# Optimization experiments

Measured on AMD Instinct MI355X. Metric: run time of the kernel, lower is better.

The kernel has to match this reference:

```python
import jax, jax.numpy as jnp
import numpy as np

N, E, D, C = 10000, 160000, 2500, 16


def setup_inputs() -> dict:
    key = jax.random.key(0)
    ks = jax.random.split(key, 12)
    s = 1.0 / np.sqrt(D)
    inp = {
        "x": jax.random.normal(ks[0], (N, D), dtype=jnp.float32),
        "edge_index": jax.random.randint(ks[1], (2, E), 0, N, dtype=jnp.int64),
        # SAGEConv 1 (mean aggregator): out = x @ W_self + mean_neigh @ W_neigh + b
        "W1_self": jax.random.normal(ks[2], (D, D), dtype=jnp.float32) * s,
        "W1_neigh": jax.random.normal(ks[3], (D, D), dtype=jnp.float32) * s,
        "b1": jnp.zeros((D,), dtype=jnp.float32),
        # SAGEConv 2
        "W2_self": jax.random.normal(ks[4], (D, D), dtype=jnp.float32) * s,
        "W2_neigh": jax.random.normal(ks[5], (D, D), dtype=jnp.float32) * s,
        "b2": jnp.zeros((D,), dtype=jnp.float32),
        # classifier: Linear(D, D) -> ReLU -> Linear(D, C)
        "Wc1": jax.random.normal(ks[6], (D, D), dtype=jnp.float32) * s,
        "bc1": jnp.zeros((D,), dtype=jnp.float32),
        "Wc2": jax.random.normal(ks[7], (D, C), dtype=jnp.float32) * s,
        "bc2": jnp.zeros((C,), dtype=jnp.float32),
    }
    return inp


def _sage_conv(h, src, dst, W_self, W_neigh, b):
    # mean aggregation over in-neighbors (messages flow src -> dst)
    agg = jax.ops.segment_sum(h[src], dst, num_segments=N)          # [N, D]
    deg = jax.ops.segment_sum(jnp.ones((src.shape[0],), h.dtype), dst, num_segments=N)
    mean = agg / jnp.maximum(deg, 1.0)[:, None]
    return h @ W_self + mean @ W_neigh + b


def reference(x, edge_index, W1_self, W1_neigh, b1, W2_self, W2_neigh, b2,
              Wc1, bc1, Wc2, bc2):
    src, dst = edge_index[0], edge_index[1]
    h = jax.nn.relu(_sage_conv(x, src, dst, W1_self, W1_neigh, b1))
    h = jax.nn.relu(_sage_conv(h, src, dst, W2_self, W2_neigh, b2))
    h = jax.nn.relu(h @ Wc1 + bc1)
    return h @ Wc2 + bc2  # [N, num_classes]
```

## Files before the change

kernel.cpp:

```cpp
#include <hip/hip_runtime.h>
#include <stdint.h>

#define NNODES 10000
#define NEDGES 160000
#define DIM    2500
#define NCLS   16
#define KP     2560
#define MP     10240
#define K2     5120
#define GN     20
#define KT_SEG 40

typedef __attribute__((ext_vector_type(8))) short short8;
typedef __attribute__((ext_vector_type(4))) float f32x4;
typedef __attribute__((address_space(3))) void as3_void;
typedef const __attribute__((address_space(1))) void as1_cvoid;

__device__ __forceinline__ unsigned short f2bf(float f) {
    unsigned u = __float_as_uint(f);
    u += 0x7FFFu + ((u >> 16) & 1u);
    return (unsigned short)(u >> 16);
}
__device__ __forceinline__ float bf2f(unsigned short s) {
    return __uint_as_float(((unsigned)s) << 16);
}

__global__ void k_deg(const int* __restrict__ ei, int* __restrict__ deg) {
    int e = blockIdx.x * blockDim.x + threadIdx.x;
    if (e < NEDGES) atomicAdd(&deg[ei[NEDGES + e]], 1);
}

__global__ void k_scan(const int* __restrict__ deg, int* __restrict__ off) {
    __shared__ int s[1024];
    __shared__ int carryS;
    int t = threadIdx.x;
    if (t == 0) carryS = 0;
    __syncthreads();
    for (int c = 0; c < NNODES; c += 1024) {
        int i = c + t;
        int v = (i < NNODES) ? deg[i] : 0;
        s[t] = v;
        __syncthreads();
        for (int o = 1; o < 1024; o <<= 1) {
            int add = (t >= o) ? s[t - o] : 0;
            __syncthreads();
            s[t] += add;
            __syncthreads();
        }
        int base = carryS;
        if (i < NNODES) off[i] = base + s[t] - v;
        __syncthreads();
        if (t == 1023) carryS += s[1023];
        __syncthreads();
    }
    if (t == 0) off[NNODES] = carryS;
}

__global__ void k_fill(const int* __restrict__ ei, const int* __restrict__ off,
                       int* __restrict__ cur, int* __restrict__ csr) {
    int e = blockIdx.x * blockDim.x + threadIdx.x;
    if (e < NEDGES) {
        int s = ei[e];
        int d = ei[NEDGES + e];
        int p = atomicAdd(&cur[d], 1);
        csr[off[d] + p] = s;
    }
}

__global__ void k_cvt_x(const float* __restrict__ x,
                        unsigned short* __restrict__ hi, unsigned short* __restrict__ lo) {
    long long idx = (long long)blockIdx.x * blockDim.x + threadIdx.x;
    const int C4 = KP / 4;
    if (idx >= (long long)MP * C4) return;
    int row = (int)(idx / C4), c4 = (int)(idx % C4);
    int k = c4 * 4;
    float vv[4] = {0.f, 0.f, 0.f, 0.f};
    if (row < NNODES && k < DIM) {
        float4 v = *(const float4*)(x + (size_t)row * DIM + k);
        vv[0] = v.x; vv[1] = v.y; vv[2] = v.z; vv[3] = v.w;
    }
    unsigned hw[2], lw[2];
    for (int j = 0; j < 2; j++) {
        unsigned short h0 = f2bf(vv[2*j]);     unsigned short l0 = f2bf(vv[2*j]   - bf2f(h0));
        unsigned short h1 = f2bf(vv[2*j+1]);   unsigned short l1 = f2bf(vv[2*j+1] - bf2f(h1));
        hw[j] = (unsigned)h0 | ((unsigned)h1 << 16);
        lw[j] = (unsigned)l0 | ((unsigned)l1 << 16);
    }
    *(uint2*)(hi + (size_t)row * KP + k) = make_uint2(hw[0], hw[1]);
    *(uint2*)(lo + (size_t)row * KP + k) = make_uint2(lw[0], lw[1]);
}

__global__ __launch_bounds__(320) void k_agg(
    const unsigned short* __restrict__ shi, const unsigned short* __restrict__ slo,
    const int* __restrict__ off, const int* __restrict__ csr, const int* __restrict__ deg,
    unsigned short* __restrict__ mhi, unsigned short* __restrict__ mlo) {
    int d = blockIdx.x;
    int t = threadIdx.x;
    int s0 = off[d], s1 = off[d + 1];
    float acc[8];
    #pragma unroll
    for (int i = 0; i < 8; i++) acc[i] = 0.f;
    for (int e = s0; e < s1; e++) {
        int s = csr[e];
        uint4 hv = *((const uint4*)(shi + (size_t)s * KP) + t);
        uint4 lv = *((const uint4*)(slo + (size_t)s * KP) + t);
        unsigned hu[4] = {hv.x, hv.y, hv.z, hv.w};
        unsigned lu[4] = {lv.x, lv.y, lv.z, lv.w};
        #pragma unroll
        for (int j = 0; j < 4; j++) {
            acc[2*j]   += bf2f((unsigned short)(hu[j] & 0xFFFFu)) + bf2f((unsigned short)(lu[j] & 0xFFFFu));
            acc[2*j+1] += bf2f((unsigned short)(hu[j] >> 16))     + bf2f((unsigned short)(lu[j] >> 16));
        }
    }
    int dg = deg[d];
    float inv = 1.0f / (float)(dg > 1 ? dg : 1);
    unsigned oh[4], ol[4];
    #pragma unroll
    for (int j = 0; j < 4; j++) {
        float m0 = acc[2*j] * inv, m1 = acc[2*j+1] * inv;
        unsigned short h0 = f2bf(m0); unsigned short l0 = f2bf(m0 - bf2f(h0));
        unsigned short h1 = f2bf(m1); unsigned short l1 = f2bf(m1 - bf2f(h1));
        oh[j] = (unsigned)h0 | ((unsigned)h1 << 16);
        ol[j] = (unsigned)l0 | ((unsigned)l1 << 16);
    }
    *((uint4*)(mhi + (size_t)d * KP) + t) = make_uint4(oh[0], oh[1], oh[2], oh[3]);
    *((uint4*)(mlo + (size_t)d * KP) + t) = make_uint4(ol[0], ol[1], ol[2], ol[3]);
}

__global__ __launch_bounds__(256) void k_cvt_w(const float* __restrict__ W,
                                               unsigned short* __restrict__ wth,
                                               unsigned short* __restrict__ wtl, int seg) {
    __shared__ float tile[64][65];
    int k0 = blockIdx.x * 64, n0 = blockIdx.y * 64;
    int t = threadIdx.x;
    for (int j = 0; j < 16; j++) {
        int lin = t + j * 256;
        int kk = lin >> 6, nn = lin & 63;
        int gk = k0 + kk, gn = n0 + nn;
        tile[kk][nn] = (gk < DIM && gn < DIM) ? W[(size_t)gk * DIM + gn] : 0.f;
    }
    __syncthreads();
    for (int j = 0; j < 16; j++) {
        int lin = t + j * 256;
        int nn = lin >> 6, kk = lin & 63;
        float v = tile[kk][nn];
        unsigned short h = f2bf(v);
        unsigned short l = f2bf(v - bf2f(h));
        size_t o = (size_t)(n0 + nn) * K2 + (size_t)seg * KP + (k0 + kk);
        wth[o] = h;
        wtl[o] = l;
    }
}

__global__ __launch_bounds__(256, 2) void k_gemm(
    const unsigned short* __restrict__ AsH, const unsigned short* __restrict__ AsL,
    const unsigned short* __restrict__ AmH, const unsigned short* __restrict__ AmL,
    const unsigned short* __restrict__ BH,  const unsigned short* __restrict__ BL,
    const float* __restrict__ bias,
    unsigned short* __restrict__ OH, unsigned short* __restrict__ OL, int ktiles) {
    __shared__ __align__(16) unsigned short lds[4 * 128 * 64];
    const int tid = threadIdx.x;
    const int wave = tid >> 6, lane = tid & 63;
    const int g = blockIdx.x;
    const int tm = g / GN, tn = g % GN;

    const int srow = tid >> 3;
    const int sc = (tid & 7) ^ (srow & 7);
    size_t aOff[4], bOff[4];
    #pragma unroll
    for (int j = 0; j < 4; j++) {
        int row = j * 32 + srow;
        aOff[j] = (size_t)(tm * 128 + row) * KP + sc * 8;
        bOff[j] = (size_t)(tn * 128 + row) * K2 + sc * 8;
    }
    char* ldsB = (char*)lds;
    const int dstBase = wave * 1024;

    const int wr = wave >> 1, wc = wave & 1;
    const int frow = lane & 15, fk = lane >> 4;
    int aFo[2][4], bFo[2][4];
    #pragma unroll
    for (int s = 0; s < 2; s++) {
        #pragma unroll
        for (int i = 0; i < 4; i++) {
            int ra = wr * 64 + i * 16 + frow;
            aFo[s][i] = ra * 64 + (((s * 4 + fk) ^ (ra & 7)) * 8);
            int rb = wc * 64 + i * 16 + frow;
            bFo[s][i] = rb * 64 + (((s * 4 + fk) ^ (rb & 7)) * 8);
        }
    }

    f32x4 acc[4][4];
    #pragma unroll
    for (int i = 0; i < 4; i++)
        #pragma unroll
        for (int j = 0; j < 4; j++) acc[i][j] = (f32x4){0.f, 0.f, 0.f, 0.f};

    for (int kt = 0; kt < ktiles; kt++) {
        const unsigned short *Ah, *Al;
        int kA;
        if (kt < KT_SEG) { Ah = AsH; Al = AsL; kA = kt * 64; }
        else             { Ah = AmH; Al = AmL; kA = (kt - KT_SEG) * 64; }
        const int kB = kt * 64;
        #pragma unroll
        for (int j = 0; j < 4; j++) {
            __builtin_amdgcn_global_load_lds((as1_cvoid*)(Ah + aOff[j] + kA),
                (as3_void*)(ldsB + 0 * 16384 + j * 4096 + dstBase), 16, 0, 0);
            __builtin_amdgcn_global_load_lds((as1_cvoid*)(Al + aOff[j] + kA),
                (as3_void*)(ldsB + 1 * 16384 + j * 4096 + dstBase), 16, 0, 0);
            __builtin_amdgcn_global_load_lds((as1_cvoid*)(BH + bOff[j] + kB),
                (as3_void*)(ldsB + 2 * 16384 + j * 4096 + dstBase), 16, 0, 0);
            __builtin_amdgcn_global_load_lds((as1_cvoid*)(BL + bOff[j] + kB),
                (as3_void*)(ldsB + 3 * 16384 + j * 4096 + dstBase), 16, 0, 0);
        }
        __syncthreads();
        #pragma unroll
        for (int s = 0; s < 2; s++) {
            short8 ah[4], al[4], bh[4], bl[4];
            #pragma unroll
            for (int i = 0; i < 4; i++) {
                ah[i] = *(const short8*)&lds[0 * 8192 + aFo[s][i]];
                al[i] = *(const short8*)&lds[1 * 8192 + aFo[s][i]];
                bh[i] = *(const short8*)&lds[2 * 8192 + bFo[s][i]];
                bl[i] = *(const short8*)&lds[3 * 8192 + bFo[s][i]];
            }
            #pragma unroll
            for (int mi = 0; mi < 4; mi++)
                #pragma unroll
                for (int ni = 0; ni < 4; ni++) {
                    acc[mi][ni] = __builtin_amdgcn_mfma_f32_16x16x32_bf16(ah[mi], bh[ni], acc[mi][ni], 0, 0, 0);
                    acc[mi][ni] = __builtin_amdgcn_mfma_f32_16x16x32_bf16(ah[mi], bl[ni], acc[mi][ni], 0, 0, 0);
                    acc[mi][ni] = __builtin_amdgcn_mfma_f32_16x16x32_bf16(al[mi], bh[ni], acc[mi][ni], 0, 0, 0);
                }
        }
        __syncthreads();
    }

    const int r4 = (lane >> 4) * 4;
    #pragma unroll
    for (int ni = 0; ni < 4; ni++) {
        int gn = tn * 128 + wc * 64 + ni * 16 + (lane & 15);
        bool valid = gn < DIM;
        float bv = valid ? bias[gn] : 0.f;
        #pragma unroll
        for (int mi = 0; mi < 4; mi++) {
            int gmBase = tm * 128 + wr * 64 + mi * 16 + r4;
            #pragma unroll
            for (int rg = 0; rg < 4; rg++) {
                float v = acc[mi][ni][rg] + bv;
                v = fmaxf(v, 0.f);
                if (!valid) v = 0.f;
                size_t o = (size_t)(gmBase + rg) * KP + gn;
                unsigned short h = f2bf(v);
                OH[o] = h;
                OL[o] = f2bf(v - bf2f(h));
            }
        }
    }
}

__global__ __launch_bounds__(256) void k_head(
    const unsigned short* __restrict__ HH, const unsigned short* __restrict__ HL,
    const float* __restrict__ W, const float* __restrict__ b, float* __restrict__ out) {
    const int m = blockIdx.x;
    const int t = threadIdx.x;
    const unsigned short* rh = HH + (size_t)m * KP;
    const unsigned short* rl = HL + (size_t)m * KP;
    float acc[NCLS];
    #pragma unroll
    for (int c = 0; c < NCLS; c++) acc[c] = 0.f;
    for (int j = 0; j < 5; j++) {
        int k0 = (j * 256 + t) * 2;
        if (k0 >= DIM) continue;
        unsigned hv = *(const unsigned*)(rh + k0);
        unsigned lv = *(const unsigned*)(rl + k0);
        float v0 = bf2f((unsigned short)(hv & 0xFFFFu)) + bf2f((unsigned short)(lv & 0xFFFFu));
        float v1 = bf2f((unsigned short)(hv >> 16)) + bf2f((unsigned short)(lv >> 16));
        const float* w0 = W + (size_t)k0 * NCLS;
        #pragma unroll
        for (int c = 0; c < NCLS; c++) acc[c] += v0 * w0[c] + v1 * w0[NCLS + c];
    }
    #pragma unroll
    for (int o = 32; o > 0; o >>= 1)
        #pragma unroll
        for (int c = 0; c < NCLS; c++) acc[c] += __shfl_down(acc[c], o);
    __shared__ float red[4][NCLS];
    if ((t & 63) == 0)
        #pragma unroll
        for (int c = 0; c < NCLS; c++) red[t >> 6][c] = acc[c];
    __syncthreads();
    if (t < NCLS)
        out[(size_t)m * NCLS + t] = red[0][t] + red[1][t] + red[2][t] + red[3][t] + b[t];
}

extern "C" void kernel_launch(void* const* d_in, const int* in_sizes, int n_in,
                              void* d_out, int out_size, void* d_ws, size_t ws_size,
                              hipStream_t stream) {
    const float* x   = (const float*)d_in[0];
    const int* ei    = (const int*)d_in[1];
    const float* W1s = (const float*)d_in[2];
    const float* W1n = (const float*)d_in[3];
    const float* b1  = (const float*)d_in[4];
    const float* W2s = (const float*)d_in[5];
    const float* W2n = (const float*)d_in[6];
    const float* b2  = (const float*)d_in[7];
    const float* Wc1 = (const float*)d_in[8];
    const float* bc1 = (const float*)d_in[9];
    const float* Wc2 = (const float*)d_in[10];
    const float* bc2 = (const float*)d_in[11];

    char* p = (char*)d_ws;
    auto nxt = [&](size_t bytes) -> char* {
        char* r = p;
        p += (bytes + 255) & ~(size_t)255;
        return r;
    };
    const size_t PLB = (size_t)MP * KP * sizeof(unsigned short);
    unsigned short* F0H = (unsigned short*)nxt(PLB);
    unsigned short* F0L = (unsigned short*)nxt(PLB);
    unsigned short* F1H = (unsigned short*)nxt(PLB);
    unsigned short* F1L = (unsigned short*)nxt(PLB);
    unsigned short* FMH = (unsigned short*)nxt(PLB);
    unsigned short* FML = (unsigned short*)nxt(PLB);
    const size_t WTB = (size_t)KP * K2 * sizeof(unsigned short);
    unsigned short* WTH = (unsigned short*)nxt(WTB);
    unsigned short* WTL = (unsigned short*)nxt(WTB);
    int* deg = (int*)nxt(NNODES * 4);
    int* off = (int*)nxt((NNODES + 1) * 4);
    int* cur = (int*)nxt(NNODES * 4);
    int* csr = (int*)nxt(NEDGES * 4);

    hipMemsetAsync(deg, 0, NNODES * 4, stream);
    hipMemsetAsync(cur, 0, NNODES * 4, stream);

    k_deg<<<(NEDGES + 255) / 256, 256, 0, stream>>>(ei, deg);
    k_scan<<<1, 1024, 0, stream>>>(deg, off);
    k_fill<<<(NEDGES + 255) / 256, 256, 0, stream>>>(ei, off, cur, csr);

    k_cvt_x<<<(int)(((size_t)MP * (KP / 4) + 255) / 256), 256, 0, stream>>>(x, F0H, F0L);

    k_agg<<<NNODES, 320, 0, stream>>>(F0H, F0L, off, csr, deg, FMH, FML);
    k_cvt_w<<<dim3(40, 40), 256, 0, stream>>>(W1s, WTH, WTL, 0);
    k_cvt_w<<<dim3(40, 40), 256, 0, stream>>>(W1n, WTH, WTL, 1);
    k_gemm<<<80 * GN, 256, 0, stream>>>(F0H, F0L, FMH, FML, WTH, WTL, b1, F1H, F1L, 80);

    k_agg<<<NNODES, 320, 0, stream>>>(F1H, F1L, off, csr, deg, FMH, FML);
    k_cvt_w<<<dim3(40, 40), 256, 0, stream>>>(W2s, WTH, WTL, 0);
    k_cvt_w<<<dim3(40, 40), 256, 0, stream>>>(W2n, WTH, WTL, 1);
    k_gemm<<<80 * GN, 256, 0, stream>>>(F1H, F1L, FMH, FML, WTH, WTL, b2, F0H, F0L, 80);

    k_cvt_w<<<dim3(40, 40), 256, 0, stream>>>(Wc1, WTH, WTL, 0);
    k_gemm<<<80 * GN, 256, 0, stream>>>(F0H, F0L, F0H, F0L, WTH, WTL, bc1, F1H, F1L, 40);

    k_head<<<NNODES, 256, 0, stream>>>(F1H, F1L, Wc2, bc2, (float*)d_out);
}
```

Measured before the change: 3.039 ms.

## Rewrite split-bf16 GEMM as 256x256 double-buffered pipelined kernel with sweeps

The GEMM moves to 256x256 tiles with 512 threads and a 128KB double-buffered LDS ring. Global-to-LDS loads for the next stage are interleaved across four sub-phases, with explicit vmcnt waits, barriers and setprio around the MFMA blocks. The three bf16 hi/lo product terms now run as three separate sweeps over K instead of three MFMAs per fragment. This gives more data reuse per tile and lets loads overlap compute. The neighbour aggregation loop is also unrolled by two edges to get more loads in flight. In exchange the grid shrinks to 400 blocks, occupancy drops, and the hand-placed waitcnt scheduling is fragile.

New measurement: 3.172 ms. 4.4% more time.

```diff
diff --git a/kernel.cpp b/kernel.cpp
--- a/kernel.cpp
+++ b/kernel.cpp
@@ -8,13 +8,13 @@
 #define KP     2560
 #define MP     10240
 #define K2     5120
-#define GN     20
 #define KT_SEG 40
 
 typedef __attribute__((ext_vector_type(8))) short short8;
 typedef __attribute__((ext_vector_type(4))) float f32x4;
 typedef __attribute__((address_space(3))) void as3_void;
 typedef const __attribute__((address_space(1))) void as1_cvoid;
+typedef unsigned short ushort_t;
 
 __device__ __forceinline__ unsigned short f2bf(float f) {
     unsigned u = __float_as_uint(f);
@@ -100,7 +100,26 @@
     float acc[8];
     #pragma unroll
     for (int i = 0; i < 8; i++) acc[i] = 0.f;
-    for (int e = s0; e < s1; e++) {
+    int e = s0;
+    for (; e + 2 <= s1; e += 2) {
+        int sa = csr[e], sb = csr[e + 1];
+        uint4 ha = *((const uint4*)(shi + (size_t)sa * KP) + t);
+        uint4 la = *((const uint4*)(slo + (size_t)sa * KP) + t);
+        uint4 hb = *((const uint4*)(shi + (size_t)sb * KP) + t);
+        uint4 lb = *((const uint4*)(slo + (size_t)sb * KP) + t);
+        unsigned hua[4] = {ha.x, ha.y, ha.z, ha.w};
+        unsigned lua[4] = {la.x, la.y, la.z, la.w};
+        unsigned hub[4] = {hb.x, hb.y, hb.z, hb.w};
+        unsigned lub[4] = {lb.x, lb.y, lb.z, lb.w};
+        #pragma unroll
+        for (int j = 0; j < 4; j++) {
+            acc[2*j]   += bf2f((unsigned short)(hua[j] & 0xFFFFu)) + bf2f((unsigned short)(lua[j] & 0xFFFFu))
+                        + bf2f((unsigned short)(hub[j] & 0xFFFFu)) + bf2f((unsigned short)(lub[j] & 0xFFFFu));
+            acc[2*j+1] += bf2f((unsigned short)(hua[j] >> 16))     + bf2f((unsigned short)(lua[j] >> 16))
+                        + bf2f((unsigned short)(hub[j] >> 16))     + bf2f((unsigned short)(lub[j] >> 16));
+        }
+    }
+    for (; e < s1; e++) {
         int s = csr[e];
         uint4 hv = *((const uint4*)(shi + (size_t)s * KP) + t);
         uint4 lv = *((const uint4*)(slo + (size_t)s * KP) + t);
@@ -152,111 +171,175 @@
     }
 }
 
-__global__ __launch_bounds__(256, 2) void k_gemm(
-    const unsigned short* __restrict__ AsH, const unsigned short* __restrict__ AsL,
-    const unsigned short* __restrict__ AmH, const unsigned short* __restrict__ AmL,
-    const unsigned short* __restrict__ BH,  const unsigned short* __restrict__ BL,
+__global__ __launch_bounds__(512) void k_gemm(
+    const ushort_t* __restrict__ AsH, const ushort_t* __restrict__ AsL,
+    const ushort_t* __restrict__ AmH, const ushort_t* __restrict__ AmL,
+    const ushort_t* __restrict__ BH,  const ushort_t* __restrict__ BL,
     const float* __restrict__ bias,
-    unsigned short* __restrict__ OH, unsigned short* __restrict__ OL, int ktiles) {
-    __shared__ __align__(16) unsigned short lds[4 * 128 * 64];
-    const int tid = threadIdx.x;
-    const int wave = tid >> 6, lane = tid & 63;
-    const int g = blockIdx.x;
-    const int tm = g / GN, tn = g % GN;
-
-    const int srow = tid >> 3;
-    const int sc = (tid & 7) ^ (srow & 7);
-    size_t aOff[4], bOff[4];
-    #pragma unroll
-    for (int j = 0; j < 4; j++) {
-        int row = j * 32 + srow;
-        aOff[j] = (size_t)(tm * 128 + row) * KP + sc * 8;
-        bOff[j] = (size_t)(tn * 128 + row) * K2 + sc * 8;
-    }
-    char* ldsB = (char*)lds;
-    const int dstBase = wave * 1024;
-
-    const int wr = wave >> 1, wc = wave & 1;
-    const int frow = lane & 15, fk = lane >> 4;
-    int aFo[2][4], bFo[2][4];
-    #pragma unroll
-    for (int s = 0; s < 2; s++) {
-        #pragma unroll
-        for (int i = 0; i < 4; i++) {
-            int ra = wr * 64 + i * 16 + frow;
-            aFo[s][i] = ra * 64 + (((s * 4 + fk) ^ (ra & 7)) * 8);
-            int rb = wc * 64 + i * 16 + frow;
-            bFo[s][i] = rb * 64 + (((s * 4 + fk) ^ (rb & 7)) * 8);
-        }
-    }
-
-    f32x4 acc[4][4];
-    #pragma unroll
-    for (int i = 0; i < 4; i++)
+    ushort_t* __restrict__ OH, ushort_t* __restrict__ OL,
+    int nt, int ktSweep) {
+    __shared__ __align__(16) ushort_t lds[65536];
+    char* ldsByte = (char*)lds;
+    const int tid  = threadIdx.x;
+    const int lane = tid & 63, wave = tid >> 6;
+    const int wr = wave >> 2, wc = wave & 3;
+    const int frow = lane & 15, fk = (lane >> 4) & 3;
+    const int tm = blockIdx.x / 10, tn = blockIdx.x % 10;
+
+    const int sr = tid >> 3;
+    const int sc = tid & 7;
+    const int swz = sc ^ (sr & 7);
+    const unsigned offA0 = (unsigned)(tm*256 +   0 + sr) * KP + swz*8;
+    const unsigned offA1 = (unsigned)(tm*256 + 128 + sr) * KP + swz*8;
+    const unsigned offA4 = (unsigned)(tm*256 +  64 + sr) * KP + swz*8;
+    const unsigned offA5 = (unsigned)(tm*256 + 192 + sr) * KP + swz*8;
+    auto bsrc = [&](int rL) {
+        int np = rL >> 7, q = (rL >> 5) & 3, w = rL & 31;
+        int r = q*64 + np*32 + w;
+        return (unsigned)(tn*256 + r) * K2 + (unsigned)(sc ^ (rL & 7)) * 8;
+    };
+    const unsigned offB2 = bsrc(  0 + sr);
+    const unsigned offB3 = bsrc( 64 + sr);
+    const unsigned offB6 = bsrc(128 + sr);
+    const unsigned offB7 = bsrc(192 + sr);
+    const int waveB = wave << 10;
+
+    const int q8 = frow & 7;
+    int aB[2], bB[2];
+    #pragma unroll
+    for (int kk = 0; kk < 2; kk++) {
+        aB[kk] = (wr*128 + frow)*128 + (((kk*4+fk) ^ q8) << 4);
+        bB[kk] = 32768 + (wc*32 + frow)*128 + (((kk*4+fk) ^ q8) << 4);
+    }
+
+    f32x4 acc[8][4];
+    #pragma unroll
+    for (int i = 0; i < 8; i++)
         #pragma unroll
         for (int j = 0; j < 4; j++) acc[i][j] = (f32x4){0.f, 0.f, 0.f, 0.f};
 
-    for (int kt = 0; kt < ktiles; kt++) {
-        const unsigned short *Ah, *Al;
-        int kA;
-        if (kt < KT_SEG) { Ah = AsH; Al = AsL; kA = kt * 64; }
-        else             { Ah = AmH; Al = AmL; kA = (kt - KT_SEG) * 64; }
-        const int kB = kt * 64;
-        #pragma unroll
-        for (int j = 0; j < 4; j++) {
-            __builtin_amdgcn_global_load_lds((as1_cvoid*)(Ah + aOff[j] + kA),
-                (as3_void*)(ldsB + 0 * 16384 + j * 4096 + dstBase), 16, 0, 0);
-            __builtin_amdgcn_global_load_lds((as1_cvoid*)(Al + aOff[j] + kA),
-                (as3_void*)(ldsB + 1 * 16384 + j * 4096 + dstBase), 16, 0, 0);
-            __builtin_amdgcn_global_load_lds((as1_cvoid*)(BH + bOff[j] + kB),
-                (as3_void*)(ldsB + 2 * 16384 + j * 4096 + dstBase), 16, 0, 0);
-            __builtin_amdgcn_global_load_lds((as1_cvoid*)(BL + bOff[j] + kB),
-                (as3_void*)(ldsB + 3 * 16384 + j * 4096 + dstBase), 16, 0, 0);
-        }
-        __syncthreads();
-        #pragma unroll
-        for (int s = 0; s < 2; s++) {
-            short8 ah[4], al[4], bh[4], bl[4];
+    int sweep = 0, kks = 0;
+    const ushort_t *Ap, *Bp; int kcA, kcB;
+#define SET_STAGE() do { \
+        const ushort_t* Ah_ = (kks < KT_SEG) ? AsH : AmH; \
+        const ushort_t* Al_ = (kks < KT_SEG) ? AsL : AmL; \
+        Ap = (sweep < 2) ? Ah_ : Al_; \
+        Bp = (sweep == 1) ? BL : BH; \
+        kcA = ((kks < KT_SEG) ? kks : kks - KT_SEG) * 64; \
+        kcB = kks * 64; } while (0)
+    SET_STAGE();
+
+#define GLD(OFF, PTR, KC, DSTB) \
+    __builtin_amdgcn_global_load_lds((as1_cvoid*)((PTR) + (OFF) + (unsigned)(KC)), \
+        (as3_void*)(ldsByte + (DSTB) + waveB), 16, 0, 0)
+
+    GLD(offA0, Ap, kcA, 0);           GLD(offA1, Ap, kcA, 16384);
+    GLD(offB2, Bp, kcB, 32768);       GLD(offB3, Bp, kcB, 32768 + 8192);
+    GLD(offA4, Ap, kcA, 8192);        GLD(offA5, Ap, kcA, 24576);
+    GLD(offB6, Bp, kcB, 32768+16384); GLD(offB7, Bp, kcB, 32768+24576);
+
+#define FRAG_READS(MP, NP) \
+    short8 af[4][2], bf[2][2]; \
+    _Pragma("unroll") \
+    for (int kk = 0; kk < 2; kk++) { \
+        _Pragma("unroll") \
+        for (int i = 0; i < 4; i++) \
+            af[i][kk] = *(const short8*)(ldsByte + bufByte + aB[kk] + ((MP)*4 + i) * 2048); \
+        _Pragma("unroll") \
+        for (int j = 0; j < 2; j++) \
+            bf[j][kk] = *(const short8*)(ldsByte + bufByte + bB[kk] + (NP)*16384 + j*2048); \
+    }
+
+#define MFMA16(MP, NP) \
+    _Pragma("unroll") \
+    for (int kk = 0; kk < 2; kk++) \
+        _Pragma("unroll") \
+        for (int i = 0; i < 4; i++) \
+            _Pragma("unroll") \
+            for (int j = 0; j < 2; j++) \
+                acc[(MP)*4+i][(NP)*2+j] = __builtin_amdgcn_mfma_f32_16x16x32_bf16( \
+                    af[i][kk], bf[j][kk], acc[(MP)*4+i][(NP)*2+j], 0, 0, 0);
+
+#define PH_TAIL() \
+    asm volatile("s_waitcnt lgkmcnt(0)" ::: "memory"); \
+    __builtin_amdgcn_sched_barrier(0); \
+    __builtin_amdgcn_s_setprio(1)
+
+    for (int t = 0; t < nt; t++) {
+        const int bufByte = (t & 1) << 16;
+        const int stg = 65536 - bufByte;
+        const bool doStage = (t + 1 < nt);
+        if (doStage) {
+            kks++; if (kks == ktSweep) { kks = 0; sweep++; }
+            SET_STAGE();
+        }
+        {
+            asm volatile("s_waitcnt vmcnt(4)" ::: "memory");
+            asm volatile("s_barrier" ::: "memory");
+            FRAG_READS(0, 0);
+            if (doStage) { GLD(offA0, Ap, kcA, stg + 0); GLD(offA1, Ap, kcA, stg + 16384); }
+            PH_TAIL();
+            MFMA16(0, 0);
+            __builtin_amdgcn_s_setprio(0);
+        }
+        {
+            if (doStage) asm volatile("s_waitcnt vmcnt(4)" ::: "memory");
+            else         asm volatile("s_waitcnt vmcnt(2)" ::: "memory");
+            asm volatile("s_barrier" ::: "memory");
+            FRAG_READS(1, 0);
+            if (doStage) { GLD(offB2, Bp, kcB, stg + 32768); GLD(offB3, Bp, kcB, stg + 32768 + 8192); }
+            PH_TAIL();
+            MFMA16(1, 0);
+            __builtin_amdgcn_s_setprio(0);
+        }
+        {
+            if (doStage) asm volatile("s_waitcnt vmcnt(4)" ::: "memory");
+            else         asm volatile("s_waitcnt vmcnt(0)" ::: "memory");
+            asm volatile("s_barrier" ::: "memory");
+            FRAG_READS(1, 1);
+            if (doStage) { GLD(offA4, Ap, kcA, stg + 8192); GLD(offA5, Ap, kcA, stg + 24576); }
+            PH_TAIL();
+            MFMA16(1, 1);
+            __builtin_amdgcn_s_setprio(0);
+        }
+        {
+            asm volatile("s_barrier" ::: "memory");
+            FRAG_READS(0, 1);
+            if (doStage) { GLD(offB6, Bp, kcB, stg + 32768+16384); GLD(offB7, Bp, kcB, stg + 32768+24576); }
+            PH_TAIL();
+            MFMA16(0, 1);
+            __builtin_amdgcn_s_setprio(0);
+        }
+    }
+
+    #pragma unroll
+    for (int np = 0; np < 2; np++)
+        #pragma unroll
+        for (int nj = 0; nj < 2; nj++) {
+            int ni = np*2 + nj;
+            int gn = tn*256 + wc*64 + ni*16 + frow;
+            bool valid = gn < DIM;
+            float bv = valid ? bias[gn] : 0.f;
             #pragma unroll
-            for (int i = 0; i < 4; i++) {
-                ah[i] = *(const short8*)&lds[0 * 8192 + aFo[s][i]];
-                al[i] = *(const short8*)&lds[1 * 8192 + aFo[s][i]];
-                bh[i] = *(const short8*)&lds[2 * 8192 + bFo[s][i]];
-                bl[i] = *(const short8*)&lds[3 * 8192 + bFo[s][i]];
+            for (int mi = 0; mi < 8; mi++) {
+                int gmBase = tm*256 + wr*128 + mi*16 + ((lane >> 4) & 3) * 4;
+                #pragma unroll
+                for (int rg = 0; rg < 4; rg++) {
+                    float v = acc[mi][ni][rg] + bv;
+                    v = fmaxf(v, 0.f);
+                    if (!valid) v = 0.f;
+                    size_t o = (size_t)(gmBase + rg) * KP + gn;
+                    unsigned short h = f2bf(v);
+                    OH[o] = h;
+                    OL[o] = f2bf(v - bf2f(h));
+                }
             }
-            #pragma unroll
-            for (int mi = 0; mi < 4; mi++)
-                #pragma unroll
-                for (int ni = 0; ni < 4; ni++) {
-                    acc[mi][ni] = __builtin_amdgcn_mfma_f32_16x16x32_bf16(ah[mi], bh[ni], acc[mi][ni], 0, 0, 0);
-                    acc[mi][ni] = __builtin_amdgcn_mfma_f32_16x16x32_bf16(ah[mi], bl[ni], acc[mi][ni], 0, 0, 0);
-                    acc[mi][ni] = __builtin_amdgcn_mfma_f32_16x16x32_bf16(al[mi], bh[ni], acc[mi][ni], 0, 0, 0);
-                }
-        }
-        __syncthreads();
-    }
-
-    const int r4 = (lane >> 4) * 4;
-    #pragma unroll
-    for (int ni = 0; ni < 4; ni++) {
-        int gn = tn * 128 + wc * 64 + ni * 16 + (lane & 15);
-        bool valid = gn < DIM;
-        float bv = valid ? bias[gn] : 0.f;
-        #pragma unroll
-        for (int mi = 0; mi < 4; mi++) {
-            int gmBase = tm * 128 + wr * 64 + mi * 16 + r4;
-            #pragma unroll
-            for (int rg = 0; rg < 4; rg++) {
-                float v = acc[mi][ni][rg] + bv;
-                v = fmaxf(v, 0.f);
-                if (!valid) v = 0.f;
-                size_t o = (size_t)(gmBase + rg) * KP + gn;
-                unsigned short h = f2bf(v);
-                OH[o] = h;
-                OL[o] = f2bf(v - bf2f(h));
-            }
-        }
-    }
+        }
+#undef SET_STAGE
+#undef GLD
+#undef FRAG_READS
+#undef MFMA16
+#undef PH_TAIL
 }
 
 __global__ __launch_bounds__(256) void k_head(
@@ -342,15 +425,15 @@
     k_agg<<<NNODES, 320, 0, stream>>>(F0H, F0L, off, csr, deg, FMH, FML);
     k_cvt_w<<<dim3(40, 40), 256, 0, stream>>>(W1s, WTH, WTL, 0);
     k_cvt_w<<<dim3(40, 40), 256, 0, stream>>>(W1n, WTH, WTL, 1);
-    k_gemm<<<80 * GN, 256, 0, stream>>>(F0H, F0L, FMH, FML, WTH, WTL, b1, F1H, F1L, 80);
+    k_gemm<<<400, 512, 0, stream>>>(F0H, F0L, FMH, FML, WTH, WTL, b1, F1H, F1L, 240, 80);
 
     k_agg<<<NNODES, 320, 0, stream>>>(F1H, F1L, off, csr, deg, FMH, FML);
     k_cvt_w<<<dim3(40, 40), 256, 0, stream>>>(W2s, WTH, WTL, 0);
     k_cvt_w<<<dim3(40, 40), 256, 0, stream>>>(W2n, WTH, WTL, 1);
-    k_gemm<<<80 * GN, 256, 0, stream>>>(F1H, F1L, FMH, FML, WTH, WTL, b2, F0H, F0L, 80);
+    k_gemm<<<400, 512, 0, stream>>>(F1H, F1L, FMH, FML, WTH, WTL, b2, F0H, F0L, 240, 80);
 
     k_cvt_w<<<dim3(40, 40), 256, 0, stream>>>(Wc1, WTH, WTL, 0);
-    k_gemm<<<80 * GN, 256, 0, stream>>>(F0H, F0L, F0H, F0L, WTH, WTL, bc1, F1H, F1L, 40);
+    k_gemm<<<400, 512, 0, stream>>>(F0H, F0L, F0H, F0L, WTH, WTL, bc1, F1H, F1L, 120, 40);
 
     k_head<<<NNODES, 256, 0, stream>>>(F1H, F1L, Wc2, bc2, (float*)d_out);
 }
```
